# Performance work log

Hardware: AMD Instinct MI355X
Metric: run time of the kernel (lower is better)

## Reference

```python
import jax, jax.numpy as jnp
import numpy as np

T = 32400   # bs*H*W BEV queries (1*180*180)
S = 16896   # bs*num_cams*h*w image keys (1*6*32*88)
E = 256     # embed_dim
H = 8       # num_heads
D = 32      # head_dim
MAXL = 32   # max interval length (ref_num_f)


def _mlp(x, w1, b1, w2, b2):
    # nn.Sequential(Linear(E,2E), ReLU, Linear(2E,E))
    return jax.nn.relu(x @ w1 + b1) @ w2 + b2


def setup_inputs() -> dict:
    k0 = jax.random.key(0)
    ks = jax.random.split(k0, 8)
    # ragged interval structure: every BEV cell has an interval of length (idx%32)+1
    lengths = (np.arange(T) % MAXL) + 1
    starts = np.concatenate([np.zeros(1, np.int64), np.cumsum(lengths)[:-1]])
    N = int(lengths.sum())  # 534472 frustum points
    ranks_bev = np.repeat(np.arange(T), lengths)          # sorted by BEV cell
    rng = np.random.default_rng(0)
    ranks_feat = rng.integers(0, S, size=N)               # which key/value row each point reads

    def lin(k, fi, fo):
        return jax.random.normal(k, (fi, fo), jnp.float32) * (1.0 / np.sqrt(fi))

    key_feat = jax.random.normal(ks[1], (S, E), jnp.float32)
    return dict(
        query_depth=jax.random.normal(ks[0], (T, E), jnp.float32),
        key=key_feat,
        value=key_feat,  # module asserts torch.equal(key, value)
        q_w1=lin(ks[2], E, 2 * E), q_b1=jnp.zeros((2 * E,), jnp.float32),
        q_w2=lin(ks[3], 2 * E, E), q_b2=jnp.zeros((E,), jnp.float32),
        k_w1=lin(ks[4], E, 2 * E), k_b1=jnp.zeros((2 * E,), jnp.float32),
        k_w2=lin(ks[5], 2 * E, E), k_b2=jnp.zeros((E,), jnp.float32),
        ranks_feat_f=jnp.asarray(ranks_feat, jnp.int32),
        ranks_bev_f=jnp.asarray(ranks_bev, jnp.int32),
        interval_starts_f=jnp.asarray(starts, jnp.int32),
        interval_lengths_f=jnp.asarray(lengths, jnp.int32),
        ref_num=MAXL,
    )


def reference(query_depth, key, value,
              q_w1, q_b1, q_w2, q_b2,
              k_w1, k_b1, k_w2, k_b2,
              ranks_feat_f, ranks_bev_f,
              interval_starts_f, interval_lengths_f, ref_num):
    scaling = 1.0 / jnp.sqrt(jnp.float32(D))
    q = (_mlp(query_depth, q_w1, q_b1, q_w2, q_b2) * scaling).reshape(T, H, D)
    k = _mlp(key, k_w1, k_b1, k_w2, k_b2).reshape(S, H, D)
    v = value.reshape(S, H, D)

    N = ranks_bev_f.shape[0]
    pt = jnp.arange(N, dtype=jnp.int32)
    # interval id of each point (intervals are contiguous, sorted by start)
    iid = jnp.searchsorted(interval_starts_f, pt, side='right') - 1
    ranks_ref = pt - interval_starts_f[iid]  # within-interval slot, in [0, ref_num)

    # per-point raw attention logit: q[bev] . k[feat] per head  -> [N, H]
    w = jnp.einsum('nhd,nhd->nh', q[ranks_bev_f], k[ranks_feat_f])

    # scatter into ragged weight tensor [T, H, ref_num]; padding masked to -1e9
    attn = jnp.full((T, H, ref_num), -1e9, jnp.float32)
    attn = attn.at[ranks_bev_f, :, ranks_ref].set(w)
    attn = jax.nn.softmax(attn, axis=-1)

    # gather normalized weights back per point and scatter-combine values
    wp = attn[ranks_bev_f, :, ranks_ref]          # [N, H]
    vp = v[ranks_feat_f]                          # [N, H, D]
    out = jnp.zeros((T, H, D), jnp.float32).at[ranks_bev_f].add(wp[:, :, None] * vp)
    return out.reshape(T, E)
```

## Files before the change

kernel.cpp:

```cpp
#include <hip/hip_runtime.h>
#include <hip/hip_bf16.h>
#include <cstdint>
#include <cstddef>

constexpr int T_Q   = 32400;
constexpr int T_PAD = 32512;
constexpr int S_K   = 16896;
constexpr int E_DIM = 256;
constexpr int HID   = 512;

typedef __bf16 bf16x8 __attribute__((ext_vector_type(8)));
typedef float  f32x4  __attribute__((ext_vector_type(4)));
typedef unsigned short ushort8v __attribute__((ext_vector_type(8)));

__device__ __forceinline__ void async16(const __hip_bfloat16* gp, __hip_bfloat16* lp) {
    __builtin_amdgcn_global_load_lds(
        (const __attribute__((address_space(1))) void*)(gp),
        (__attribute__((address_space(3))) void*)(lp), 16, 0, 0);
}

__device__ __forceinline__ float b2f(unsigned short u) {
    return __uint_as_float(((unsigned)u) << 16);
}

constexpr int NB_Q = (T_PAD * E_DIM / 4) / 256;
constexpr int NB_K = (S_K * E_DIM / 4) / 256;
constexpr int NB_PREP = NB_Q + NB_K + NB_K + 128;

__global__ __launch_bounds__(256) void prep(
    const float* __restrict__ q_in, const float* __restrict__ key_in,
    const float* __restrict__ val_in,
    const float* __restrict__ s0, const float* __restrict__ s1,
    const float* __restrict__ s2, const float* __restrict__ s3,
    __hip_bfloat16* __restrict__ qA, __hip_bfloat16* __restrict__ kA,
    __hip_bfloat16* __restrict__ kvB,
    __hip_bfloat16* __restrict__ d0, __hip_bfloat16* __restrict__ d1,
    __hip_bfloat16* __restrict__ d2, __hip_bfloat16* __restrict__ d3) {
    __shared__ float tb[64][65];
    const int b = blockIdx.x;
    const int tid = threadIdx.x;

    if (b < NB_Q + 2 * NB_K) {
        const float* src;
        int bl, valid, isv = 0;
        if (b < NB_Q) { src = q_in; bl = b; valid = T_Q * E_DIM; }
        else if (b < NB_Q + NB_K) { src = key_in; bl = b - NB_Q; valid = S_K * E_DIM; }
        else { src = val_in; bl = b - NB_Q - NB_K; valid = S_K * E_DIM; isv = 1; }
        int i = (bl * 256 + tid) * 4;
        float4 f = make_float4(0.f, 0.f, 0.f, 0.f);
        if (i < valid) f = *(const float4*)(src + i);
        union { ushort4 u4; __hip_bfloat16 bb[4]; } cv;
        cv.bb[0] = __float2bfloat16(f.x);
        cv.bb[1] = __float2bfloat16(f.y);
        cv.bb[2] = __float2bfloat16(f.z);
        cv.bb[3] = __float2bfloat16(f.w);
        if (isv) {
            int r = i >> 8, c = i & 255;
            *(ushort4*)(kvB + (size_t)r * 512 + 256 + c) = cv.u4;
        } else {
            __hip_bfloat16* dst = (b < NB_Q) ? qA : kA;
            *(ushort4*)(dst + i) = cv.u4;
        }
        return;
    }

    int tloc = b - (NB_Q + 2 * NB_K);
    int m = tloc >> 5;
    int tt = tloc & 31;
    const float* S = m == 0 ? s0 : m == 1 ? s1 : m == 2 ? s2 : s3;
    __hip_bfloat16* D = m == 0 ? d0 : m == 1 ? d1 : m == 2 ? d2 : d3;
    int Kd, Nd, kt, nt;
    if ((m & 1) == 0) { Kd = 256; Nd = 512; kt = tt & 3; nt = tt >> 2; }
    else              { Kd = 512; Nd = 256; kt = tt & 7; nt = tt >> 3; }
    int tx = tid & 63, ty = tid >> 6;
#pragma unroll
    for (int p = 0; p < 16; ++p) {
        int row = ty * 16 + p;
        tb[row][tx] = S[(size_t)(kt * 64 + row) * Nd + nt * 64 + tx];
    }
    __syncthreads();
#pragma unroll
    for (int p = 0; p < 16; ++p) {
        int row = ty * 16 + p;
        D[(size_t)(nt * 64 + row) * Kd + kt * 64 + tx] = __float2bfloat16(tb[tx][row]);
    }
}

constexpr int BM = 128, BN = 128, BK = 32;

__global__ __launch_bounds__(256) void gemm_dual(
    const __hip_bfloat16* __restrict__ Aq, const __hip_bfloat16* __restrict__ Ak,
    const __hip_bfloat16* __restrict__ BTq, const __hip_bfloat16* __restrict__ BTk,
    const float* __restrict__ biasq, const float* __restrict__ biask,
    __hip_bfloat16* __restrict__ Cq, __hip_bfloat16* __restrict__ Ck,
    int K, int N, int ldcq, int ldck, int relu,
    float scaleq, float scalek, int qtiles) {
    __shared__ __hip_bfloat16 As[BM * BK];
    __shared__ __hip_bfloat16 Bs[BN * BK];

    const int ntiles = N >> 7;
    const int tm = blockIdx.x / ntiles;
    const int tn = blockIdx.x - tm * ntiles;
    const bool isq = tm < qtiles;
    const __hip_bfloat16* A  = isq ? Aq : Ak;
    const __hip_bfloat16* BT = isq ? BTq : BTk;
    const float* bias = isq ? biasq : biask;
    __hip_bfloat16* C = isq ? Cq : Ck;
    const int ldc = isq ? ldcq : ldck;
    const float scale = isq ? scaleq : scalek;
    const size_t m0 = (size_t)(isq ? tm : tm - qtiles) * BM;
    const int n0 = tn * BN;

    const int tid = threadIdx.x;
    const int w = tid >> 6, l = tid & 63;
    const int lm = l & 15, lq = l >> 4;
    const int wm = (w >> 1) << 6, wn = (w & 1) << 6;

    const int srow = l >> 2;
    const int scol = (((l & 3) ^ (srow & 3)) << 3);

    f32x4 acc[4][4] = {};

    for (int k0 = 0; k0 < K; k0 += BK) {
#pragma unroll
        for (int c = 0; c < 2; ++c) {
            int r = c * 64 + w * 16 + srow;
            async16(A  + (m0 + r) * K + k0 + scol, As + (c * 64 + w * 16) * BK);
            async16(BT + (size_t)(n0 + r) * K + k0 + scol, Bs + (c * 64 + w * 16) * BK);
        }
        __syncthreads();

        const int rsw = ((lq ^ (lm & 3)) << 3);
        bf16x8 af[4], bfr[4];
#pragma unroll
        for (int mi = 0; mi < 4; ++mi)
            af[mi] = *(const bf16x8*)(As + (wm + mi * 16 + lm) * BK + rsw);
#pragma unroll
        for (int ni = 0; ni < 4; ++ni)
            bfr[ni] = *(const bf16x8*)(Bs + (wn + ni * 16 + lm) * BK + rsw);
#pragma unroll
        for (int mi = 0; mi < 4; ++mi)
#pragma unroll
            for (int ni = 0; ni < 4; ++ni)
                acc[mi][ni] = __builtin_amdgcn_mfma_f32_16x16x32_bf16(
                    af[mi], bfr[ni], acc[mi][ni], 0, 0, 0);
        __syncthreads();
    }

#pragma unroll
    for (int ni = 0; ni < 4; ++ni) {
        int col = n0 + wn + ni * 16 + lm;
        float bv = bias[col];
#pragma unroll
        for (int mi = 0; mi < 4; ++mi) {
            size_t rowb = m0 + wm + mi * 16 + lq * 4;
#pragma unroll
            for (int r = 0; r < 4; ++r) {
                float vv = acc[mi][ni][r] + bv;
                if (relu) vv = fmaxf(vv, 0.f);
                C[(rowb + r) * ldc + col] = __float2bfloat16(vv * scale);
            }
        }
    }
}

__global__ __launch_bounds__(256) void attn_kernel(
    const __hip_bfloat16* __restrict__ q,
    const __hip_bfloat16* __restrict__ kv,
    const int* __restrict__ rf,
    const int* __restrict__ starts,
    const int* __restrict__ lens,
    float* __restrict__ out) {
    int t = blockIdx.x * 4 + (threadIdx.x >> 6);
    if (t >= T_Q) return;
    int l = threadIdx.x & 63;
    int half = l >> 5, sub = l & 31;
    int su = __builtin_amdgcn_readfirstlane(starts[t]);
    int L  = __builtin_amdgcn_readfirstlane(lens[t]);
    int nC = (L + 1) >> 1;

    int li = l < L - 1 ? l : L - 1;
    int myf = rf[su + li];

    const char* base = (const char*)kv;
    unsigned voff[16];
#pragma unroll
    for (int c = 0; c < 16; ++c) {
        int f = __shfl(myf, 2 * c + half);
        voff[c] = ((unsigned)f << 10) + (unsigned)(sub << 4);
    }

    ushort8v qu = *(const ushort8v*)(q + (size_t)t * 256 + sub * 8);
    float qf[8];
#pragma unroll
    for (int i = 0; i < 8; ++i) qf[i] = b2f(qu[i]);

    ushort8v kb[16], vb[16];
#pragma unroll
    for (int c = 0; c < 16; ++c)
        if (c < nC) kb[c] = *(const ushort8v*)(base + voff[c]);

    float w[16];
#pragma unroll
    for (int c = 0; c < 16; ++c) w[c] = -1e30f;
#pragma unroll
    for (int c = 0; c < 16; ++c) {
        if (c < nC) {
            vb[c] = *(const ushort8v*)(base + voff[c] + 512);
            float wv = 0.f;
#pragma unroll
            for (int i = 0; i < 8; ++i) wv = fmaf(qf[i], b2f(kb[c][i]), wv);
            wv += __shfl_xor(wv, 1);
            wv += __shfl_xor(wv, 2);
            w[c] = (2 * c + half < L) ? wv : -1e30f;
        }
    }

    float mx = -1e30f;
#pragma unroll
    for (int c = 0; c < 16; ++c) mx = fmaxf(mx, w[c]);
    mx = fmaxf(mx, __shfl_xor(mx, 32));
    float s = 0.f;
#pragma unroll
    for (int c = 0; c < 16; ++c) { w[c] = __expf(w[c] - mx); s += w[c]; }
    s += __shfl_xor(s, 32);

    float a[8] = {0.f, 0.f, 0.f, 0.f, 0.f, 0.f, 0.f, 0.f};
#pragma unroll
    for (int c = 0; c < 16; ++c) {
        if (c < nC) {
#pragma unroll
            for (int i = 0; i < 8; ++i) a[i] = fmaf(w[c], b2f(vb[c][i]), a[i]);
        }
    }
#pragma unroll
    for (int i = 0; i < 8; ++i) a[i] += __shfl_xor(a[i], 32);

    float inv = 1.f / s;
    float4 o;
    o.x = (half ? a[4] : a[0]) * inv;
    o.y = (half ? a[5] : a[1]) * inv;
    o.z = (half ? a[6] : a[2]) * inv;
    o.w = (half ? a[7] : a[3]) * inv;
    *(float4*)(out + (size_t)t * 256 + sub * 8 + half * 4) = o;
}

extern "C" void kernel_launch(void* const* d_in, const int* in_sizes, int n_in,
                              void* d_out, int out_size, void* d_ws, size_t ws_size,
                              hipStream_t stream) {
    const float* q_in   = (const float*)d_in[0];
    const float* key_in = (const float*)d_in[1];
    const float* val_in = (const float*)d_in[2];
    const float* q_w1   = (const float*)d_in[3];
    const float* q_b1   = (const float*)d_in[4];
    const float* q_w2   = (const float*)d_in[5];
    const float* q_b2   = (const float*)d_in[6];
    const float* k_w1   = (const float*)d_in[7];
    const float* k_b1   = (const float*)d_in[8];
    const float* k_w2   = (const float*)d_in[9];
    const float* k_b2   = (const float*)d_in[10];
    const int* ranks_feat = (const int*)d_in[11];
    const int* starts     = (const int*)d_in[13];
    const int* lens       = (const int*)d_in[14];
    float* out = (float*)d_out;

    char* ws = (char*)d_ws;
    size_t off = 0;
    auto alloc = [&](size_t bytes) {
        char* p = ws + off;
        off += (bytes + 255) & ~(size_t)255;
        return p;
    };
    __hip_bfloat16* qA   = (__hip_bfloat16*)alloc((size_t)T_PAD * E_DIM * 2);
    __hip_bfloat16* hidQ = (__hip_bfloat16*)alloc((size_t)T_PAD * HID * 2);
    __hip_bfloat16* qMl  = (__hip_bfloat16*)alloc((size_t)T_PAD * E_DIM * 2);
    __hip_bfloat16* kA   = (__hip_bfloat16*)alloc((size_t)S_K * E_DIM * 2);
    __hip_bfloat16* hidK = (__hip_bfloat16*)alloc((size_t)S_K * HID * 2);
    __hip_bfloat16* kvB  = (__hip_bfloat16*)alloc((size_t)S_K * 512 * 2);
    __hip_bfloat16* w1qT = (__hip_bfloat16*)alloc((size_t)HID * E_DIM * 2);
    __hip_bfloat16* w2qT = (__hip_bfloat16*)alloc((size_t)E_DIM * HID * 2);
    __hip_bfloat16* w1kT = (__hip_bfloat16*)alloc((size_t)HID * E_DIM * 2);
    __hip_bfloat16* w2kT = (__hip_bfloat16*)alloc((size_t)E_DIM * HID * 2);
    (void)ws_size; (void)n_in; (void)out_size; (void)in_sizes;

    prep<<<NB_PREP, 256, 0, stream>>>(q_in, key_in, val_in,
                                      q_w1, q_w2, k_w1, k_w2,
                                      qA, kA, kvB, w1qT, w2qT, w1kT, w2kT);

    const float qscale = 0.17677669529663687f;
    const int QT = T_PAD / 128;
    const int KT = S_K / 128;

    gemm_dual<<<(QT + KT) * (HID / 128), 256, 0, stream>>>(
        qA, kA, w1qT, w1kT, q_b1, k_b1, hidQ, hidK,
        E_DIM, HID, HID, HID, 1, 1.0f, 1.0f, QT);
    gemm_dual<<<(QT + KT) * (E_DIM / 128), 256, 0, stream>>>(
        hidQ, hidK, w2qT, w2kT, q_b2, k_b2, qMl, kvB,
        HID, E_DIM, E_DIM, 512, 0, qscale, 1.0f, QT);

    attn_kernel<<<T_Q / 4, 256, 0, stream>>>(qMl, kvB, ranks_feat, starts, lens, out);
}
```

Measured before the change: 319.2 us.

## Fuse fp32-to-bf16 input cast into GEMM1, retile GEMMs, online-softmax attention

Removes the separate q/key fp32-to-bf16 conversion pass from prep and instead converts A rows to bf16 while loading them in the first MLP GEMM. Both MLP GEMMs are retiled to 64x256 output tiles with a BK of 64 and an 8-way XOR swizzle, and GEMM2 covers the full N per block. The attention kernel is rewritten to process one point per iteration across the whole wave, using online softmax with a 6-deep register prefetch ring instead of loading all keys and values up front. This trades extra exp and shuffle work per point and a serial dependency chain for lower register pressure and one fewer global round trip over the inputs.

```diff
diff --git a/kernel.cpp b/kernel.cpp
--- a/kernel.cpp
+++ b/kernel.cpp
@@ -23,16 +23,13 @@
     return __uint_as_float(((unsigned)u) << 16);
 }
 
-constexpr int NB_Q = (T_PAD * E_DIM / 4) / 256;
 constexpr int NB_K = (S_K * E_DIM / 4) / 256;
-constexpr int NB_PREP = NB_Q + NB_K + NB_K + 128;
+constexpr int NB_PREP = NB_K + 128;
 
 __global__ __launch_bounds__(256) void prep(
-    const float* __restrict__ q_in, const float* __restrict__ key_in,
     const float* __restrict__ val_in,
     const float* __restrict__ s0, const float* __restrict__ s1,
     const float* __restrict__ s2, const float* __restrict__ s3,
-    __hip_bfloat16* __restrict__ qA, __hip_bfloat16* __restrict__ kA,
     __hip_bfloat16* __restrict__ kvB,
     __hip_bfloat16* __restrict__ d0, __hip_bfloat16* __restrict__ d1,
     __hip_bfloat16* __restrict__ d2, __hip_bfloat16* __restrict__ d3) {
@@ -40,31 +37,20 @@
     const int b = blockIdx.x;
     const int tid = threadIdx.x;
 
-    if (b < NB_Q + 2 * NB_K) {
-        const float* src;
-        int bl, valid, isv = 0;
-        if (b < NB_Q) { src = q_in; bl = b; valid = T_Q * E_DIM; }
-        else if (b < NB_Q + NB_K) { src = key_in; bl = b - NB_Q; valid = S_K * E_DIM; }
-        else { src = val_in; bl = b - NB_Q - NB_K; valid = S_K * E_DIM; isv = 1; }
-        int i = (bl * 256 + tid) * 4;
-        float4 f = make_float4(0.f, 0.f, 0.f, 0.f);
-        if (i < valid) f = *(const float4*)(src + i);
+    if (b < NB_K) {
+        int i = (b * 256 + tid) * 4;
+        float4 f = *(const float4*)(val_in + i);
         union { ushort4 u4; __hip_bfloat16 bb[4]; } cv;
         cv.bb[0] = __float2bfloat16(f.x);
         cv.bb[1] = __float2bfloat16(f.y);
         cv.bb[2] = __float2bfloat16(f.z);
         cv.bb[3] = __float2bfloat16(f.w);
-        if (isv) {
-            int r = i >> 8, c = i & 255;
-            *(ushort4*)(kvB + (size_t)r * 512 + 256 + c) = cv.u4;
-        } else {
-            __hip_bfloat16* dst = (b < NB_Q) ? qA : kA;
-            *(ushort4*)(dst + i) = cv.u4;
-        }
+        int r = i >> 8, c = i & 255;
+        *(ushort4*)(kvB + (size_t)r * 512 + 256 + c) = cv.u4;
         return;
     }
 
-    int tloc = b - (NB_Q + 2 * NB_K);
+    int tloc = b - NB_K;
     int m = tloc >> 5;
     int tt = tloc & 31;
     const float* S = m == 0 ? s0 : m == 1 ? s1 : m == 2 ? s2 : s3;
@@ -86,83 +72,220 @@
     }
 }
 
-constexpr int BM = 128, BN = 128, BK = 32;
-
-__global__ __launch_bounds__(256) void gemm_dual(
+
+__global__ __launch_bounds__(256) void gemm1(
+    const float* __restrict__ Aq, const float* __restrict__ Ak,
+    const __hip_bfloat16* __restrict__ BTq, const __hip_bfloat16* __restrict__ BTk,
+    const float* __restrict__ biasq, const float* __restrict__ biask,
+    __hip_bfloat16* __restrict__ Cq, __hip_bfloat16* __restrict__ Ck,
+    int qtiles) {
+    __shared__ __hip_bfloat16 As[64 * 64];
+    __shared__ __hip_bfloat16 Bs[256 * 64];
+
+    const int tm = blockIdx.x >> 1;
+    const int tn = blockIdx.x & 1;
+    const bool isq = tm < qtiles;
+    const float* A  = isq ? Aq : Ak;
+    const __hip_bfloat16* BT = isq ? BTq : BTk;
+    const float* bias = isq ? biasq : biask;
+    __hip_bfloat16* C = isq ? Cq : Ck;
+    const int mrow0 = (isq ? tm : tm - qtiles) * 64;
+    const int rowlim = isq ? T_Q : S_K;
+    const int n0 = tn * 256;
+
+    const int tid = threadIdx.x;
+    const int w = tid >> 6, l = tid & 63;
+    const int lm = l & 15, lq = l >> 4;
+    const int wn = w * 64;
+    const int srow8 = l >> 3;
+    const int u8 = l & 7;
+    const int pu8 = u8 ^ srow8;
+    const int scolB = (u8 ^ srow8) << 3;
+
+    f32x4 acc[4][4] = {};
+
+    for (int k0 = 0; k0 < 256; k0 += 64) {
+#pragma unroll
+        for (int c = 0; c < 2; ++c) {
+            int r = w * 16 + c * 8 + srow8;
+            int gr = mrow0 + r;
+            float4 f0 = make_float4(0.f, 0.f, 0.f, 0.f);
+            float4 f1 = make_float4(0.f, 0.f, 0.f, 0.f);
+            if (gr < rowlim) {
+                const float* ap = A + (size_t)gr * 256 + k0 + u8 * 8;
+                f0 = *(const float4*)ap;
+                f1 = *(const float4*)(ap + 4);
+            }
+            union { bf16x8 v; __hip_bfloat16 b[8]; } cv;
+            cv.b[0] = __float2bfloat16(f0.x); cv.b[1] = __float2bfloat16(f0.y);
+            cv.b[2] = __float2bfloat16(f0.z); cv.b[3] = __float2bfloat16(f0.w);
+            cv.b[4] = __float2bfloat16(f1.x); cv.b[5] = __float2bfloat16(f1.y);
+            cv.b[6] = __float2bfloat16(f1.z); cv.b[7] = __float2bfloat16(f1.w);
+            *(bf16x8*)(As + r * 64 + pu8 * 8) = cv.v;
+        }
+#pragma unroll
+        for (int c = 0; c < 8; ++c) {
+            int r = w * 64 + c * 8 + srow8;
+            async16(BT + (size_t)(n0 + r) * 256 + k0 + scolB,
+                    Bs + (w * 64 + c * 8) * 64);
+        }
+        __syncthreads();
+
+#pragma unroll
+        for (int ks = 0; ks < 2; ++ks) {
+            bf16x8 af[4], bfr[4];
+#pragma unroll
+            for (int mi = 0; mi < 4; ++mi) {
+                int row = mi * 16 + lm;
+                int pu = (ks * 4 + lq) ^ (row & 7);
+                af[mi] = *(const bf16x8*)(As + row * 64 + pu * 8);
+            }
+#pragma unroll
+            for (int ni = 0; ni < 4; ++ni) {
+                int row = wn + ni * 16 + lm;
+                int pu = (ks * 4 + lq) ^ (row & 7);
+                bfr[ni] = *(const bf16x8*)(Bs + row * 64 + pu * 8);
+            }
+#pragma unroll
+            for (int mi = 0; mi < 4; ++mi)
+#pragma unroll
+                for (int ni = 0; ni < 4; ++ni)
+                    acc[mi][ni] = __builtin_amdgcn_mfma_f32_16x16x32_bf16(
+                        af[mi], bfr[ni], acc[mi][ni], 0, 0, 0);
+        }
+        __syncthreads();
+    }
+
+#pragma unroll
+    for (int ni = 0; ni < 4; ++ni) {
+        int col = n0 + wn + ni * 16 + lm;
+        float bv = bias[col];
+#pragma unroll
+        for (int mi = 0; mi < 4; ++mi) {
+            size_t rowb = (size_t)mrow0 + mi * 16 + lq * 4;
+#pragma unroll
+            for (int r = 0; r < 4; ++r) {
+                float vv = fmaxf(acc[mi][ni][r] + bv, 0.f);
+                C[(rowb + r) * HID + col] = __float2bfloat16(vv);
+            }
+        }
+    }
+}
+
+__global__ __launch_bounds__(256) void gemm2(
     const __hip_bfloat16* __restrict__ Aq, const __hip_bfloat16* __restrict__ Ak,
     const __hip_bfloat16* __restrict__ BTq, const __hip_bfloat16* __restrict__ BTk,
     const float* __restrict__ biasq, const float* __restrict__ biask,
     __hip_bfloat16* __restrict__ Cq, __hip_bfloat16* __restrict__ Ck,
-    int K, int N, int ldcq, int ldck, int relu,
-    float scaleq, float scalek, int qtiles) {
-    __shared__ __hip_bfloat16 As[BM * BK];
-    __shared__ __hip_bfloat16 Bs[BN * BK];
-
-    const int ntiles = N >> 7;
-    const int tm = blockIdx.x / ntiles;
-    const int tn = blockIdx.x - tm * ntiles;
+    float scaleq, int qtiles) {
+    __shared__ __hip_bfloat16 As[64 * 64];
+    __shared__ __hip_bfloat16 Bs[256 * 64];
+
+    const int tm = blockIdx.x;
     const bool isq = tm < qtiles;
     const __hip_bfloat16* A  = isq ? Aq : Ak;
     const __hip_bfloat16* BT = isq ? BTq : BTk;
     const float* bias = isq ? biasq : biask;
     __hip_bfloat16* C = isq ? Cq : Ck;
-    const int ldc = isq ? ldcq : ldck;
-    const float scale = isq ? scaleq : scalek;
-    const size_t m0 = (size_t)(isq ? tm : tm - qtiles) * BM;
-    const int n0 = tn * BN;
+    const int ldc = isq ? E_DIM : 512;
+    const float scale = isq ? scaleq : 1.0f;
+    const int mrow0 = (isq ? tm : tm - qtiles) * 64;
 
     const int tid = threadIdx.x;
     const int w = tid >> 6, l = tid & 63;
     const int lm = l & 15, lq = l >> 4;
-    const int wm = (w >> 1) << 6, wn = (w & 1) << 6;
-
-    const int srow = l >> 2;
-    const int scol = (((l & 3) ^ (srow & 3)) << 3);
+    const int wn = w * 64;
+    const int srow8 = l >> 3;
+    const int u8 = l & 7;
+    const int scol = (u8 ^ srow8) << 3;
 
     f32x4 acc[4][4] = {};
 
-    for (int k0 = 0; k0 < K; k0 += BK) {
+    for (int k0 = 0; k0 < 512; k0 += 64) {
 #pragma unroll
         for (int c = 0; c < 2; ++c) {
-            int r = c * 64 + w * 16 + srow;
-            async16(A  + (m0 + r) * K + k0 + scol, As + (c * 64 + w * 16) * BK);
-            async16(BT + (size_t)(n0 + r) * K + k0 + scol, Bs + (c * 64 + w * 16) * BK);
+            int r = w * 16 + c * 8 + srow8;
+            async16(A + (size_t)(mrow0 + r) * 512 + k0 + scol,
+                    As + (w * 16 + c * 8) * 64);
+        }
+#pragma unroll
+        for (int c = 0; c < 8; ++c) {
+            int r = w * 64 + c * 8 + srow8;
+            async16(BT + (size_t)r * 512 + k0 + scol,
+                    Bs + (w * 64 + c * 8) * 64);
         }
         __syncthreads();
 
-        const int rsw = ((lq ^ (lm & 3)) << 3);
-        bf16x8 af[4], bfr[4];
-#pragma unroll
-        for (int mi = 0; mi < 4; ++mi)
-            af[mi] = *(const bf16x8*)(As + (wm + mi * 16 + lm) * BK + rsw);
-#pragma unroll
-        for (int ni = 0; ni < 4; ++ni)
-            bfr[ni] = *(const bf16x8*)(Bs + (wn + ni * 16 + lm) * BK + rsw);
-#pragma unroll
-        for (int mi = 0; mi < 4; ++mi)
-#pragma unroll
-            for (int ni = 0; ni < 4; ++ni)
-                acc[mi][ni] = __builtin_amdgcn_mfma_f32_16x16x32_bf16(
-                    af[mi], bfr[ni], acc[mi][ni], 0, 0, 0);
+#pragma unroll
+        for (int ks = 0; ks < 2; ++ks) {
+            bf16x8 af[4], bfr[4];
+#pragma unroll
+            for (int mi = 0; mi < 4; ++mi) {
+                int row = mi * 16 + lm;
+                int pu = (ks * 4 + lq) ^ (row & 7);
+                af[mi] = *(const bf16x8*)(As + row * 64 + pu * 8);
+            }
+#pragma unroll
+            for (int ni = 0; ni < 4; ++ni) {
+                int row = wn + ni * 16 + lm;
+                int pu = (ks * 4 + lq) ^ (row & 7);
+                bfr[ni] = *(const bf16x8*)(Bs + row * 64 + pu * 8);
+            }
+#pragma unroll
+            for (int mi = 0; mi < 4; ++mi)
+#pragma unroll
+                for (int ni = 0; ni < 4; ++ni)
+                    acc[mi][ni] = __builtin_amdgcn_mfma_f32_16x16x32_bf16(
+                        af[mi], bfr[ni], acc[mi][ni], 0, 0, 0);
+        }
         __syncthreads();
     }
 
 #pragma unroll
     for (int ni = 0; ni < 4; ++ni) {
-        int col = n0 + wn + ni * 16 + lm;
+        int col = wn + ni * 16 + lm;
         float bv = bias[col];
 #pragma unroll
         for (int mi = 0; mi < 4; ++mi) {
-            size_t rowb = m0 + wm + mi * 16 + lq * 4;
+            size_t rowb = (size_t)mrow0 + mi * 16 + lq * 4;
 #pragma unroll
             for (int r = 0; r < 4; ++r) {
-                float vv = acc[mi][ni][r] + bv;
-                if (relu) vv = fmaxf(vv, 0.f);
-                C[(rowb + r) * ldc + col] = __float2bfloat16(vv * scale);
-            }
-        }
-    }
-}
+                float vv = (acc[mi][ni][r] + bv) * scale;
+                C[(rowb + r) * ldc + col] = __float2bfloat16(vv);
+            }
+        }
+    }
+}
+
+#define PREF1(BUF, C)                                                        \
+    {                                                                        \
+        int f_ = __shfl(myf, (C));                                           \
+        BUF = *(const ushort8v*)(kv + ((size_t)f_ << 9) + (l << 3));         \
+    }
+
+#define PROC1(BUF)                                                           \
+    {                                                                        \
+        float wv = 0.f;                                                      \
+        _Pragma("unroll") for (int i = 0; i < 8; ++i)                        \
+            wv = fmaf(qf[i], b2f(BUF[i]), wv);                               \
+        wv += __shfl_xor(wv, 1);                                             \
+        wv += __shfl_xor(wv, 2);                                             \
+        float t2 = __shfl_xor(wv, 32);                                       \
+        float sc = half ? t2 : wv;                                           \
+        float mn = fmaxf(m, sc);                                             \
+        float al = __expf(m - mn);                                           \
+        float p  = __expf(sc - mn);                                          \
+        m = mn;                                                              \
+        s = fmaf(s, al, p);                                                  \
+        _Pragma("unroll") for (int i = 0; i < 8; ++i)                        \
+            a[i] = fmaf(p, b2f(BUF[i]), a[i] * al);                          \
+    }
+
+#define STEP(BUF, J)                                                         \
+    if (c + (J) < L) {                                                       \
+        PROC1(BUF);                                                          \
+        if (c + (J) + 6 < L) PREF1(BUF, c + (J) + 6);                        \
+    }
 
 __global__ __launch_bounds__(256) void attn_kernel(
     const __hip_bfloat16* __restrict__ q,
@@ -177,72 +300,44 @@
     int half = l >> 5, sub = l & 31;
     int su = __builtin_amdgcn_readfirstlane(starts[t]);
     int L  = __builtin_amdgcn_readfirstlane(lens[t]);
-    int nC = (L + 1) >> 1;
 
     int li = l < L - 1 ? l : L - 1;
     int myf = rf[su + li];
 
-    const char* base = (const char*)kv;
-    unsigned voff[16];
-#pragma unroll
-    for (int c = 0; c < 16; ++c) {
-        int f = __shfl(myf, 2 * c + half);
-        voff[c] = ((unsigned)f << 10) + (unsigned)(sub << 4);
-    }
-
     ushort8v qu = *(const ushort8v*)(q + (size_t)t * 256 + sub * 8);
     float qf[8];
 #pragma unroll
     for (int i = 0; i < 8; ++i) qf[i] = b2f(qu[i]);
 
-    ushort8v kb[16], vb[16];
-#pragma unroll
-    for (int c = 0; c < 16; ++c)
-        if (c < nC) kb[c] = *(const ushort8v*)(base + voff[c]);
-
-    float w[16];
-#pragma unroll
-    for (int c = 0; c < 16; ++c) w[c] = -1e30f;
-#pragma unroll
-    for (int c = 0; c < 16; ++c) {
-        if (c < nC) {
-            vb[c] = *(const ushort8v*)(base + voff[c] + 512);
-            float wv = 0.f;
-#pragma unroll
-            for (int i = 0; i < 8; ++i) wv = fmaf(qf[i], b2f(kb[c][i]), wv);
-            wv += __shfl_xor(wv, 1);
-            wv += __shfl_xor(wv, 2);
-            w[c] = (2 * c + half < L) ? wv : -1e30f;
-        }
-    }
-
-    float mx = -1e30f;
-#pragma unroll
-    for (int c = 0; c < 16; ++c) mx = fmaxf(mx, w[c]);
-    mx = fmaxf(mx, __shfl_xor(mx, 32));
-    float s = 0.f;
-#pragma unroll
-    for (int c = 0; c < 16; ++c) { w[c] = __expf(w[c] - mx); s += w[c]; }
-    s += __shfl_xor(s, 32);
-
+    float m = -INFINITY, s = 0.f;
     float a[8] = {0.f, 0.f, 0.f, 0.f, 0.f, 0.f, 0.f, 0.f};
-#pragma unroll
-    for (int c = 0; c < 16; ++c) {
-        if (c < nC) {
-#pragma unroll
-            for (int i = 0; i < 8; ++i) a[i] = fmaf(w[c], b2f(vb[c][i]), a[i]);
-        }
-    }
-#pragma unroll
-    for (int i = 0; i < 8; ++i) a[i] += __shfl_xor(a[i], 32);
-
-    float inv = 1.f / s;
-    float4 o;
-    o.x = (half ? a[4] : a[0]) * inv;
-    o.y = (half ? a[5] : a[1]) * inv;
-    o.z = (half ? a[6] : a[2]) * inv;
-    o.w = (half ? a[7] : a[3]) * inv;
-    *(float4*)(out + (size_t)t * 256 + sub * 8 + half * 4) = o;
+
+    ushort8v b0 = {}, b1 = {}, b2 = {}, b3 = {}, b4 = {}, b5 = {};
+    PREF1(b0, 0);
+    if (L > 1) PREF1(b1, 1);
+    if (L > 2) PREF1(b2, 2);
+    if (L > 3) PREF1(b3, 3);
+    if (L > 4) PREF1(b4, 4);
+    if (L > 5) PREF1(b5, 5);
+
+    for (int c = 0; c < L; c += 6) {
+        STEP(b0, 0)
+        STEP(b1, 1)
+        STEP(b2, 2)
+        STEP(b3, 3)
+        STEP(b4, 4)
+        STEP(b5, 5)
+    }
+
+    if (half) {
+        float inv = 1.f / s;
+        float* op = out + (size_t)t * 256 + sub * 8;
+        float4 o0, o1;
+        o0.x = a[0] * inv; o0.y = a[1] * inv; o0.z = a[2] * inv; o0.w = a[3] * inv;
+        o1.x = a[4] * inv; o1.y = a[5] * inv; o1.z = a[6] * inv; o1.w = a[7] * inv;
+        *(float4*)op = o0;
+        *(float4*)(op + 4) = o1;
+    }
 }
 
 extern "C" void kernel_launch(void* const* d_in, const int* in_sizes, int n_in,
@@ -271,11 +366,9 @@
         off += (bytes + 255) & ~(size_t)255;
         return p;
     };
-    __hip_bfloat16* qA   = (__hip_bfloat16*)alloc((size_t)T_PAD * E_DIM * 2);
     __hip_bfloat16* hidQ = (__hip_bfloat16*)alloc((size_t)T_PAD * HID * 2);
+    __hip_bfloat16* hidK = (__hip_bfloat16*)alloc((size_t)S_K * HID * 2);
     __hip_bfloat16* qMl  = (__hip_bfloat16*)alloc((size_t)T_PAD * E_DIM * 2);
-    __hip_bfloat16* kA   = (__hip_bfloat16*)alloc((size_t)S_K * E_DIM * 2);
-    __hip_bfloat16* hidK = (__hip_bfloat16*)alloc((size_t)S_K * HID * 2);
     __hip_bfloat16* kvB  = (__hip_bfloat16*)alloc((size_t)S_K * 512 * 2);
     __hip_bfloat16* w1qT = (__hip_bfloat16*)alloc((size_t)HID * E_DIM * 2);
     __hip_bfloat16* w2qT = (__hip_bfloat16*)alloc((size_t)E_DIM * HID * 2);
@@ -283,20 +376,17 @@
     __hip_bfloat16* w2kT = (__hip_bfloat16*)alloc((size_t)E_DIM * HID * 2);
     (void)ws_size; (void)n_in; (void)out_size; (void)in_sizes;
 
-    prep<<<NB_PREP, 256, 0, stream>>>(q_in, key_in, val_in,
-                                      q_w1, q_w2, k_w1, k_w2,
-                                      qA, kA, kvB, w1qT, w2qT, w1kT, w2kT);
+    prep<<<NB_PREP, 256, 0, stream>>>(val_in, q_w1, q_w2, k_w1, k_w2,
+                                      kvB, w1qT, w2qT, w1kT, w2kT);
 
     const float qscale = 0.17677669529663687f;
-    const int QT = T_PAD / 128;
-    const int KT = S_K / 128;
-
-    gemm_dual<<<(QT + KT) * (HID / 128), 256, 0, stream>>>(
-        qA, kA, w1qT, w1kT, q_b1, k_b1, hidQ, hidK,
-        E_DIM, HID, HID, HID, 1, 1.0f, 1.0f, QT);
-    gemm_dual<<<(QT + KT) * (E_DIM / 128), 256, 0, stream>>>(
-        hidQ, hidK, w2qT, w2kT, q_b2, k_b2, qMl, kvB,
-        HID, E_DIM, E_DIM, 512, 0, qscale, 1.0f, QT);
+    const int QT = T_PAD / 64;
+    const int KT = S_K / 64;
+
+    gemm1<<<(QT + KT) * 2, 256, 0, stream>>>(
+        q_in, key_in, w1qT, w1kT, q_b1, k_b1, hidQ, hidK, QT);
+    gemm2<<<QT + KT, 256, 0, stream>>>(
+        hidQ, hidK, w2qT, w2kT, q_b2, k_b2, qMl, kvB, qscale, QT);
 
     attn_kernel<<<T_Q / 4, 256, 0, stream>>>(qMl, kvB, ranks_feat, starts, lens, out);
 }
```

New measurement: 293.9 us. 7.9% less time.
